# Optimization experiments

Hardware: AMD Instinct MI355X
Metric: run time of the kernel (lower is better)

The kernel has to match this reference:

```python
import jax, jax.numpy as jnp
import numpy as np
from jax import lax

EPS = 1e-5
DN = ('NCDHW', 'OIDHW', 'NCDHW')
CHANNELS = [4, 32, 64, 128, 256, 512]
OUT_CH = 256


def _conv_s2(x, w):
    # 3x3x3 conv, stride 2, padding 1 (torchsparse spnn.Conv3d on densified grid)
    return lax.conv_general_dilated(x, w, window_strides=(2, 2, 2),
                                    padding=[(1, 1)] * 3, dimension_numbers=DN)


def _bn_relu(x, g, b, m, v):
    # inference BatchNorm (running stats) + ReLU, fused elementwise
    inv = g * lax.rsqrt(v + EPS)           # [C]
    shp = (1, -1, 1, 1, 1)
    return jnp.maximum(x * inv.reshape(shp) + (b - m * inv).reshape(shp), 0.0)


def setup_inputs() -> dict:
    key = jax.random.key(0)
    ks = jax.random.split(key, 32)
    inp = {}
    inp['x'] = jax.random.normal(ks[0], (2, 4, 128, 128, 128), dtype=jnp.float32)
    ki = 1
    for i in range(5):
        cin, cout = CHANNELS[i], CHANNELS[i + 1]
        fan_in = cin * 27
        inp[f'w{i+1}'] = jax.random.normal(ks[ki], (cout, cin, 3, 3, 3), dtype=jnp.float32) / np.sqrt(fan_in); ki += 1
        inp[f'g{i+1}'] = 1.0 + 0.1 * jax.random.normal(ks[ki], (cout,), dtype=jnp.float32); ki += 1
        inp[f'b{i+1}'] = 0.1 * jax.random.normal(ks[ki], (cout,), dtype=jnp.float32); ki += 1
        inp[f'm{i+1}'] = 0.1 * jax.random.normal(ks[ki], (cout,), dtype=jnp.float32); ki += 1
        inp[f'v{i+1}'] = jax.random.uniform(ks[ki], (cout,), dtype=jnp.float32, minval=0.5, maxval=1.5); ki += 1
    inp['w_out'] = jax.random.normal(ks[ki], (OUT_CH, 512, 1, 1, 1), dtype=jnp.float32) / np.sqrt(512.0)
    return inp


def reference(x, w1, g1, b1, m1, v1, w2, g2, b2, m2, v2, w3, g3, b3, m3, v3,
              w4, g4, b4, m4, v4, w5, g5, b5, m5, v5, w_out):
    h = _bn_relu(_conv_s2(x, w1), g1, b1, m1, v1)   # [B,32,64,64,64]
    h = _bn_relu(_conv_s2(h, w2), g2, b2, m2, v2)   # [B,64,32,32,32]
    h = _bn_relu(_conv_s2(h, w3), g3, b3, m3, v3)   # [B,128,16,16,16]
    h = _bn_relu(_conv_s2(h, w4), g4, b4, m4, v4)   # [B,256,8,8,8]
    h = _bn_relu(_conv_s2(h, w5), g5, b5, m5, v5)   # [B,512,4,4,4]
    # 1x1x1 output conv, stride 1
    out = lax.conv_general_dilated(h, w_out, window_strides=(1, 1, 1),
                                   padding=[(0, 0)] * 3, dimension_numbers=DN)
    return out  # [B,256,4,4,4]
```

## Files before the change

kernel.cpp:

```cpp
#include <hip/hip_runtime.h>

static constexpr float kEps = 1e-5f;

using bf16x8 = __attribute__((ext_vector_type(8))) short;
using f32x4 = __attribute__((ext_vector_type(4))) float;
using f32x2 = __attribute__((ext_vector_type(2))) float;

constexpr int ilog2(int n) { return n <= 1 ? 0 : 1 + ilog2(n / 2); }

__device__ inline unsigned bf_rne(float v) {
  unsigned u = __float_as_uint(v);
  return (u + 0x7FFFu + ((u >> 16) & 1u)) >> 16;
}
__device__ inline void split_bf(float v, unsigned short& h, unsigned short& l) {
  unsigned hb = bf_rne(v);
  h = (unsigned short)hb;
  float hf = __uint_as_float(hb << 16);
  l = (unsigned short)bf_rne(v - hf);
}

__device__ inline void pk_fma(f32x2& d, f32x2 a, f32x2 b) {
  asm volatile("v_pk_fma_f32 %0, %1, %2, %0" : "+v"(d) : "v"(a), "v"(b));
}

__device__ inline void repack_s1_body(int idx, const float* __restrict__ w,
                                      const float* __restrict__ g,
                                      const float* __restrict__ b,
                                      const float* __restrict__ m,
                                      const float* __restrict__ v,
                                      float* __restrict__ wT,
                                      float* __restrict__ bias) {
  constexpr int CIN = 4, COUT = 32, total = COUT * CIN * 27;
  if (idx < COUT) {
    float inv = g[idx] * rsqrtf(v[idx] + kEps);
    bias[idx] = b[idx] - m[idx] * inv;
  }
  if (idx < total) {
    int cout = idx % COUT;
    int ck = idx / COUT;
    int cin = ck / 27;
    int k = ck % 27;
    float inv = g[cout] * rsqrtf(v[cout] + kEps);
    wT[idx] = w[(cout * CIN + cin) * 27 + k] * inv;
  }
}

template <int CIN, int COUT>
__device__ inline void repack_bf_body(int idx, const float* __restrict__ w,
                                      const float* __restrict__ g,
                                      const float* __restrict__ b,
                                      const float* __restrict__ m,
                                      const float* __restrict__ v,
                                      unsigned short* __restrict__ wh,
                                      unsigned short* __restrict__ wl,
                                      float* __restrict__ bias) {
  constexpr int total = 27 * COUT * CIN;
  constexpr int LC = ilog2(CIN), LO = ilog2(COUT);
  if (idx < COUT) {
    float inv = g[idx] * rsqrtf(v[idx] + kEps);
    bias[idx] = b[idx] - m[idx] * inv;
  }
  if (idx < total) {
    int ci = idx & (CIN - 1);
    int t = idx >> LC;
    int co = t & (COUT - 1);
    int tap = t >> LO;
    float inv = g[co] * rsqrtf(v[co] + kEps);
    float val = w[((size_t)co * CIN + ci) * 27 + tap] * inv;
    unsigned short h, l;
    split_bf(val, h, l);
    wh[idx] = h;
    wl[idx] = l;
  }
}

__global__ __launch_bounds__(256) void repack_all(
    const float* w1, const float* g1, const float* b1, const float* m1, const float* v1,
    const float* w2, const float* g2, const float* b2, const float* m2, const float* v2,
    const float* w3, const float* g3, const float* b3, const float* m3, const float* v3,
    const float* w4, const float* g4, const float* b4, const float* m4, const float* v4,
    const float* w5, const float* g5, const float* b5, const float* m5, const float* v5,
    const float* w_out, float* wt1, unsigned short* w2h, unsigned short* w2l,
    unsigned short* w3h, unsigned short* w3l, unsigned short* w4h, unsigned short* w4l,
    unsigned short* w5h, unsigned short* w5l, float* woutT, float* bs1, float* bs2,
    float* bs3, float* bs4, float* bs5) {
  int blk = blockIdx.x;
  int tid = threadIdx.x;
  if (blk < 14) {
    repack_s1_body(blk * 256 + tid, w1, g1, b1, m1, v1, wt1, bs1);
  } else if (blk < 230) {
    repack_bf_body<32, 64>((blk - 14) * 256 + tid, w2, g2, b2, m2, v2, w2h, w2l, bs2);
  } else if (blk < 1094) {
    repack_bf_body<64, 128>((blk - 230) * 256 + tid, w3, g3, b3, m3, v3, w3h, w3l, bs3);
  } else if (blk < 4550) {
    repack_bf_body<128, 256>((blk - 1094) * 256 + tid, w4, g4, b4, m4, v4, w4h, w4l, bs4);
  } else if (blk < 18374) {
    repack_bf_body<256, 512>((blk - 4550) * 256 + tid, w5, g5, b5, m5, v5, w5h, w5l, bs5);
  } else {
    int idx = (blk - 18374) * 256 + tid;
    int co = idx & 255;
    int c = idx >> 8;
    woutT[idx] = w_out[(size_t)co * 512 + c];
  }
}

__global__ __launch_bounds__(256) void conv1_direct(
    const float* __restrict__ in, const float* __restrict__ wT,
    const float* __restrict__ bias, unsigned short* __restrict__ outh,
    unsigned short* __restrict__ outl) {
  constexpr int DI = 128, CIN = 4, COUT = 32;
  int tid = blockIdx.x * 256 + threadIdx.x;
  int x = tid & 63;
  int t = tid >> 6;
  int y = t & 63;
  t >>= 6;
  int z = t & 63;
  int bb = t >> 6;

  f32x2 acc[16];
#pragma unroll
  for (int i = 0; i < 16; ++i) acc[i] = (f32x2){0.f, 0.f};

  const float* inb = in + (size_t)bb * CIN * DI * DI * DI;
  for (int cin = 0; cin < CIN; ++cin) {
    const float* inc = inb + (size_t)cin * DI * DI * DI;
#pragma unroll
    for (int kz = 0; kz < 3; ++kz) {
      int iz = 2 * z + kz - 1;
      if (iz < 0) continue;
#pragma unroll
      for (int ky = 0; ky < 3; ++ky) {
        int iy = 2 * y + ky - 1;
        if (iy < 0) continue;
        const float* row = inc + ((size_t)iz * DI + iy) * DI;
        f32x2 rv = *reinterpret_cast<const f32x2*>(row + 2 * x);
        float xm = (x > 0) ? row[2 * x - 1] : 0.f;
        const float* wbase = wT + ((size_t)cin * 27 + (kz * 3 + ky) * 3) * COUT;
        {
          f32x2 xv2 = (f32x2){xm, xm};
#pragma unroll
          for (int i = 0; i < 16; ++i)
            pk_fma(acc[i], *reinterpret_cast<const f32x2*>(wbase + 2 * i), xv2);
        }
        {
          f32x2 xv2 = (f32x2){rv.x, rv.x};
#pragma unroll
          for (int i = 0; i < 16; ++i)
            pk_fma(acc[i], *reinterpret_cast<const f32x2*>(wbase + COUT + 2 * i), xv2);
        }
        {
          f32x2 xv2 = (f32x2){rv.y, rv.y};
#pragma unroll
          for (int i = 0; i < 16; ++i)
            pk_fma(acc[i], *reinterpret_cast<const f32x2*>(wbase + 2 * COUT + 2 * i), xv2);
        }
      }
    }
  }
  int pidx = (z & 1) * 4 + (y & 1) * 2 + (x & 1);
  size_t sub = (((size_t)(z >> 1) * 32) + (y >> 1)) * 32 + (x >> 1);
  size_t op = (((size_t)bb * 8 + pidx) * 32768 + sub) * COUT;
#pragma unroll
  for (int i = 0; i < COUT; ++i) {
    float r = fmaxf(acc[i >> 1][i & 1] + bias[i], 0.f);
    unsigned short h, l;
    split_bf(r, h, l);
    outh[op + i] = h;
    outl[op + i] = l;
  }
}

template <int CIN, int COUT, int DO, int SK, int MREP>
__global__ __launch_bounds__(256) void conv_mfma(
    const unsigned short* __restrict__ inh, const unsigned short* __restrict__ inl,
    const unsigned short* __restrict__ wh, const unsigned short* __restrict__ wl,
    const float* __restrict__ bias, unsigned short* __restrict__ outh,
    unsigned short* __restrict__ outl, float* __restrict__ partial) {
  constexpr int M = 2 * DO * DO * DO;
  constexpr int TAPS = 27 / SK;
  constexpr int KCPT = CIN / 32;
  constexpr int LD = ilog2(DO);
  constexpr int SUB = DO * DO * DO;

  const int lane = threadIdx.x & 63;
  const int wv = threadIdx.x >> 6;
  const int mWave = (blockIdx.x * 4 + wv) * (MREP * 16);
  const int nBase = blockIdx.y * 64;
  const int skid = blockIdx.z;
  const int mlane = lane & 15;
  const int kgrp = lane >> 4;

  int xf[MREP], yf[MREP], zf[MREP], bf_[MREP];
#pragma unroll
  for (int f = 0; f < MREP; ++f) {
    int m = mWave + f * 16 + mlane;
    xf[f] = m & (DO - 1);
    yf[f] = (m >> LD) & (DO - 1);
    zf[f] = (m >> (2 * LD)) & (DO - 1);
    bf_[f] = m >> (3 * LD);
  }

  f32x4 acc[MREP][4];
#pragma unroll
  for (int f = 0; f < MREP; ++f)
#pragma unroll
    for (int q = 0; q < 4; ++q) acc[f][q] = (f32x4){0.f, 0.f, 0.f, 0.f};

  for (int tp = 0; tp < TAPS; ++tp) {
    const int tap = skid * TAPS + tp;
    const int kz = tap / 9;
    const int kr = tap - kz * 9;
    const int ky = kr / 3;
    const int kx = kr - ky * 3;
    const int pidx = (kz != 1) * 4 + (ky != 1) * 2 + (kx != 1);
    const int dz = (kz == 0), dy = (ky == 0), dx = (kx == 0);

    const size_t woff = (size_t)tap * COUT * CIN + (size_t)(nBase + mlane) * CIN + kgrp * 8;
    const unsigned short* wbh = wh + woff;
    const unsigned short* wbl = wl + woff;

    long long aoff[MREP];
    bool valid[MREP];
#pragma unroll
    for (int f = 0; f < MREP; ++f) {
      int sx = xf[f] - dx, sy = yf[f] - dy, sz = zf[f] - dz;
      valid[f] = ((sx | sy | sz) >= 0);
      aoff[f] = ((long long)(bf_[f] * 8 + pidx) * SUB + (sz * DO + sy) * DO + sx) * CIN +
                kgrp * 8;
    }

#pragma unroll
    for (int kc = 0; kc < KCPT; ++kc) {
      bf16x8 Ah[MREP], Al[MREP];
#pragma unroll
      for (int f = 0; f < MREP; ++f) {
        Ah[f] = (bf16x8){0, 0, 0, 0, 0, 0, 0, 0};
        Al[f] = (bf16x8){0, 0, 0, 0, 0, 0, 0, 0};
        if (valid[f]) {
          Ah[f] = *reinterpret_cast<const bf16x8*>(inh + aoff[f] + kc * 32);
          Al[f] = *reinterpret_cast<const bf16x8*>(inl + aoff[f] + kc * 32);
        }
      }
#pragma unroll
      for (int nq = 0; nq < 4; ++nq) {
        bf16x8 Bh = *reinterpret_cast<const bf16x8*>(wbh + (size_t)nq * 16 * CIN + kc * 32);
        bf16x8 Bl = *reinterpret_cast<const bf16x8*>(wbl + (size_t)nq * 16 * CIN + kc * 32);
#pragma unroll
        for (int f = 0; f < MREP; ++f) {
          acc[f][nq] = __builtin_amdgcn_mfma_f32_16x16x32_bf16(Ah[f], Bh, acc[f][nq], 0, 0, 0);
          acc[f][nq] = __builtin_amdgcn_mfma_f32_16x16x32_bf16(Ah[f], Bl, acc[f][nq], 0, 0, 0);
          acc[f][nq] = __builtin_amdgcn_mfma_f32_16x16x32_bf16(Al[f], Bh, acc[f][nq], 0, 0, 0);
        }
      }
    }
  }

  if constexpr (SK == 1) {
    constexpr int HD = DO / 2;
#pragma unroll
    for (int f = 0; f < MREP; ++f) {
#pragma unroll
      for (int nq = 0; nq < 4; ++nq) {
        const int n = nBase + nq * 16 + mlane;
        const float bv = bias[n];
#pragma unroll
        for (int r = 0; r < 4; ++r) {
          const int mrow = mWave + f * 16 + kgrp * 4 + r;
          const int ox = mrow & (DO - 1);
          const int oy = (mrow >> LD) & (DO - 1);
          const int oz = (mrow >> (2 * LD)) & (DO - 1);
          const int ob = mrow >> (3 * LD);
          const int pp = (oz & 1) * 4 + (oy & 1) * 2 + (ox & 1);
          const size_t sub = (((size_t)(oz >> 1) * HD) + (oy >> 1)) * HD + (ox >> 1);
          const size_t addr = (((size_t)ob * 8 + pp) * (HD * HD * HD) + sub) * COUT + n;
          float vv = fmaxf(acc[f][nq][r] + bv, 0.f);
          unsigned short h, l;
          split_bf(vv, h, l);
          outh[addr] = h;
          outl[addr] = l;
        }
      }
    }
  } else {
#pragma unroll
    for (int f = 0; f < MREP; ++f) {
#pragma unroll
      for (int nq = 0; nq < 4; ++nq) {
        const int n = nBase + nq * 16 + mlane;
#pragma unroll
        for (int r = 0; r < 4; ++r) {
          const int mrow = mWave + f * 16 + kgrp * 4 + r;
          partial[((size_t)skid * M + mrow) * COUT + n] = acc[f][nq][r];
        }
      }
    }
  }
}

template <int COUT, int SK, int M, int DOP>
__global__ __launch_bounds__(256) void reduce_split(
    const float* __restrict__ partial, const float* __restrict__ bias,
    unsigned short* __restrict__ oh, unsigned short* __restrict__ ol) {
  constexpr int LD = ilog2(DOP);
  constexpr int HD = DOP / 2;
  int idx = blockIdx.x * 256 + threadIdx.x;
  int n = idx & (COUT - 1);
  int mrow = idx / COUT;
  float s = 0.f;
#pragma unroll
  for (int k = 0; k < SK; ++k) s += partial[(size_t)k * M * COUT + idx];
  float v = fmaxf(s + bias[n], 0.f);
  const int ox = mrow & (DOP - 1);
  const int oy = (mrow >> LD) & (DOP - 1);
  const int oz = (mrow >> (2 * LD)) & (DOP - 1);
  const int ob = mrow >> (3 * LD);
  const int pp = (oz & 1) * 4 + (oy & 1) * 2 + (ox & 1);
  const size_t sub = (((size_t)(oz >> 1) * HD) + (oy >> 1)) * HD + (ox >> 1);
  const size_t addr = (((size_t)ob * 8 + pp) * (HD * HD * HD) + sub) * COUT + n;
  unsigned short h, l;
  split_bf(v, h, l);
  oh[addr] = h;
  ol[addr] = l;
}

__global__ __launch_bounds__(256) void final_fused(
    const float* __restrict__ p5, const float* __restrict__ bias,
    const float* __restrict__ wt, float* __restrict__ out) {
  __shared__ float h[512];
  int p = blockIdx.x;
  int t = threadIdx.x;
#pragma unroll
  for (int cc = 0; cc < 2; ++cc) {
    int c = t + cc * 256;
    float s = 0.f;
#pragma unroll
    for (int k = 0; k < 27; ++k) s += p5[((size_t)k * 128 + p) * 512 + c];
    h[c] = fmaxf(s + bias[c], 0.f);
  }
  __syncthreads();
  int b = p >> 6, sp = p & 63;
  float acc = 0.f;
#pragma unroll 8
  for (int c = 0; c < 512; ++c) acc = fmaf(h[c], wt[(size_t)c * 256 + t], acc);
  out[((size_t)b * 256 + t) * 64 + sp] = acc;
}

extern "C" void kernel_launch(void* const* d_in, const int* in_sizes, int n_in,
                              void* d_out, int out_size, void* d_ws,
                              size_t ws_size, hipStream_t stream) {
  const float* x = (const float*)d_in[0];
  const float* w1 = (const float*)d_in[1];
  const float* g1 = (const float*)d_in[2];
  const float* bb1 = (const float*)d_in[3];
  const float* m1 = (const float*)d_in[4];
  const float* v1 = (const float*)d_in[5];
  const float* w2 = (const float*)d_in[6];
  const float* g2 = (const float*)d_in[7];
  const float* bb2 = (const float*)d_in[8];
  const float* m2 = (const float*)d_in[9];
  const float* v2 = (const float*)d_in[10];
  const float* w3 = (const float*)d_in[11];
  const float* g3 = (const float*)d_in[12];
  const float* bb3 = (const float*)d_in[13];
  const float* m3 = (const float*)d_in[14];
  const float* v3 = (const float*)d_in[15];
  const float* w4 = (const float*)d_in[16];
  const float* g4 = (const float*)d_in[17];
  const float* bb4 = (const float*)d_in[18];
  const float* m4 = (const float*)d_in[19];
  const float* v4 = (const float*)d_in[20];
  const float* w5 = (const float*)d_in[21];
  const float* g5 = (const float*)d_in[22];
  const float* bb5 = (const float*)d_in[23];
  const float* m5 = (const float*)d_in[24];
  const float* v5 = (const float*)d_in[25];
  const float* w_out = (const float*)d_in[26];
  (void)in_sizes; (void)n_in; (void)out_size; (void)ws_size;

  char* base = (char*)d_ws;
  size_t off = 0;
  auto take = [&](size_t bytes) {
    char* p = base + off;
    off = (off + bytes + 255) & ~(size_t)255;
    return p;
  };
  float* wt1 = (float*)take(3456 * 4);
  unsigned short* w2h = (unsigned short*)take(55296 * 2);
  unsigned short* w2l = (unsigned short*)take(55296 * 2);
  unsigned short* w3h = (unsigned short*)take(221184 * 2);
  unsigned short* w3l = (unsigned short*)take(221184 * 2);
  unsigned short* w4h = (unsigned short*)take(884736 * 2);
  unsigned short* w4l = (unsigned short*)take(884736 * 2);
  unsigned short* w5h = (unsigned short*)take(3538944 * 2);
  unsigned short* w5l = (unsigned short*)take(3538944 * 2);
  float* woutT = (float*)take(131072 * 4);
  float* bs1 = (float*)take(32 * 4);
  float* bs2 = (float*)take(64 * 4);
  float* bs3 = (float*)take(128 * 4);
  float* bs4 = (float*)take(256 * 4);
  float* bs5 = (float*)take(512 * 4);
  unsigned short* h1h = (unsigned short*)take((size_t)16777216 * 2);
  unsigned short* h1l = (unsigned short*)take((size_t)16777216 * 2);
  unsigned short* h2h = (unsigned short*)take((size_t)4194304 * 2);
  unsigned short* h2l = (unsigned short*)take((size_t)4194304 * 2);

  char* AR = (char*)h1h;
  float* p3 = (float*)AR;
  float* p4 = (float*)AR;
  float* p5 = (float*)AR;
  char* AR2 = AR + ((size_t)16 << 20);
  unsigned short* h3h = (unsigned short*)AR2;
  unsigned short* h3l = (unsigned short*)(AR2 + 2097152);
  unsigned short* h4h = (unsigned short*)(AR2 + 2 * 2097152);
  unsigned short* h4l = (unsigned short*)(AR2 + 2 * 2097152 + 524288);

  repack_all<<<18886, 256, 0, stream>>>(
      w1, g1, bb1, m1, v1, w2, g2, bb2, m2, v2, w3, g3, bb3, m3, v3,
      w4, g4, bb4, m4, v4, w5, g5, bb5, m5, v5, w_out,
      wt1, w2h, w2l, w3h, w3l, w4h, w4l, w5h, w5l, woutT,
      bs1, bs2, bs3, bs4, bs5);

  conv1_direct<<<2048, 256, 0, stream>>>(x, wt1, bs1, h1h, h1l);

  conv_mfma<32, 64, 32, 1, 2><<<dim3(512, 1, 1), 256, 0, stream>>>(
      h1h, h1l, w2h, w2l, bs2, h2h, h2l, nullptr);

  conv_mfma<64, 128, 16, 3, 2><<<dim3(64, 2, 3), 256, 0, stream>>>(
      h2h, h2l, w3h, w3l, bs3, nullptr, nullptr, p3);
  reduce_split<128, 3, 8192, 16><<<4096, 256, 0, stream>>>(p3, bs3, h3h, h3l);

  conv_mfma<128, 256, 8, 9, 1><<<dim3(16, 4, 9), 256, 0, stream>>>(
      h3h, h3l, w4h, w4l, bs4, nullptr, nullptr, p4);
  reduce_split<256, 9, 1024, 8><<<1024, 256, 0, stream>>>(p4, bs4, h4h, h4l);

  conv_mfma<256, 512, 4, 27, 1><<<dim3(2, 8, 27), 256, 0, stream>>>(
      h4h, h4l, w5h, w5l, bs5, nullptr, nullptr, p5);

  final_fused<<<128, 256, 0, stream>>>(p5, bs5, woutT, (float*)d_out);
}
```

Before: 467.0 us.

## Use scalar FMAs in conv1 and retune MREP and split-K for conv2-4

The conv1 direct kernel drops its inline-asm packed FMA and uses plain scalar fmaf over 32 accumulators, with a per-tap x load. The MFMA convs for layers 2-4 get a larger MREP (more M tiles per block, so fewer blocks), and layer 3 changes split-K from 3 to 9 with a matching reduce. The partial-sum scratch region grows so h3/h4 are placed past the larger p3 buffer. These changes trade weight reuse per block against parallelism and partial-sum traffic, and conv1 now depends on the compiler's own FMA scheduling.

```diff
diff --git a/kernel.cpp b/kernel.cpp
--- a/kernel.cpp
+++ b/kernel.cpp
@@ -17,10 +17,6 @@
   h = (unsigned short)hb;
   float hf = __uint_as_float(hb << 16);
   l = (unsigned short)bf_rne(v - hf);
-}
-
-__device__ inline void pk_fma(f32x2& d, f32x2 a, f32x2 b) {
-  asm volatile("v_pk_fma_f32 %0, %1, %2, %0" : "+v"(d) : "v"(a), "v"(b));
 }
 
 __device__ inline void repack_s1_body(int idx, const float* __restrict__ w,
@@ -117,9 +113,9 @@
   int z = t & 63;
   int bb = t >> 6;
 
-  f32x2 acc[16];
-#pragma unroll
-  for (int i = 0; i < 16; ++i) acc[i] = (f32x2){0.f, 0.f};
+  float acc[COUT];
+#pragma unroll
+  for (int i = 0; i < COUT; ++i) acc[i] = 0.f;
 
   const float* inb = in + (size_t)bb * CIN * DI * DI * DI;
   for (int cin = 0; cin < CIN; ++cin) {
@@ -133,26 +129,13 @@
         int iy = 2 * y + ky - 1;
         if (iy < 0) continue;
         const float* row = inc + ((size_t)iz * DI + iy) * DI;
-        f32x2 rv = *reinterpret_cast<const f32x2*>(row + 2 * x);
-        float xm = (x > 0) ? row[2 * x - 1] : 0.f;
-        const float* wbase = wT + ((size_t)cin * 27 + (kz * 3 + ky) * 3) * COUT;
-        {
-          f32x2 xv2 = (f32x2){xm, xm};
-#pragma unroll
-          for (int i = 0; i < 16; ++i)
-            pk_fma(acc[i], *reinterpret_cast<const f32x2*>(wbase + 2 * i), xv2);
-        }
-        {
-          f32x2 xv2 = (f32x2){rv.x, rv.x};
-#pragma unroll
-          for (int i = 0; i < 16; ++i)
-            pk_fma(acc[i], *reinterpret_cast<const f32x2*>(wbase + COUT + 2 * i), xv2);
-        }
-        {
-          f32x2 xv2 = (f32x2){rv.y, rv.y};
-#pragma unroll
-          for (int i = 0; i < 16; ++i)
-            pk_fma(acc[i], *reinterpret_cast<const f32x2*>(wbase + 2 * COUT + 2 * i), xv2);
+#pragma unroll
+        for (int kx = 0; kx < 3; ++kx) {
+          int ix = 2 * x + kx - 1;
+          float xv = (ix >= 0) ? row[ix] : 0.f;
+          const float* wp = wT + ((size_t)cin * 27 + (kz * 3 + ky) * 3 + kx) * COUT;
+#pragma unroll
+          for (int i = 0; i < COUT; ++i) acc[i] = fmaf(xv, wp[i], acc[i]);
         }
       }
     }
@@ -162,7 +145,7 @@
   size_t op = (((size_t)bb * 8 + pidx) * 32768 + sub) * COUT;
 #pragma unroll
   for (int i = 0; i < COUT; ++i) {
-    float r = fmaxf(acc[i >> 1][i & 1] + bias[i], 0.f);
+    float r = fmaxf(acc[i] + bias[i], 0.f);
     unsigned short h, l;
     split_bf(r, h, l);
     outh[op + i] = h;
@@ -408,7 +391,7 @@
   float* p3 = (float*)AR;
   float* p4 = (float*)AR;
   float* p5 = (float*)AR;
-  char* AR2 = AR + ((size_t)16 << 20);
+  char* AR2 = AR + ((size_t)40 << 20);
   unsigned short* h3h = (unsigned short*)AR2;
   unsigned short* h3l = (unsigned short*)(AR2 + 2097152);
   unsigned short* h4h = (unsigned short*)(AR2 + 2 * 2097152);
@@ -422,14 +405,14 @@
 
   conv1_direct<<<2048, 256, 0, stream>>>(x, wt1, bs1, h1h, h1l);
 
-  conv_mfma<32, 64, 32, 1, 2><<<dim3(512, 1, 1), 256, 0, stream>>>(
+  conv_mfma<32, 64, 32, 1, 4><<<dim3(256, 1, 1), 256, 0, stream>>>(
       h1h, h1l, w2h, w2l, bs2, h2h, h2l, nullptr);
 
-  conv_mfma<64, 128, 16, 3, 2><<<dim3(64, 2, 3), 256, 0, stream>>>(
+  conv_mfma<64, 128, 16, 9, 4><<<dim3(32, 2, 9), 256, 0, stream>>>(
       h2h, h2l, w3h, w3l, bs3, nullptr, nullptr, p3);
-  reduce_split<128, 3, 8192, 16><<<4096, 256, 0, stream>>>(p3, bs3, h3h, h3l);
-
-  conv_mfma<128, 256, 8, 9, 1><<<dim3(16, 4, 9), 256, 0, stream>>>(
+  reduce_split<128, 9, 8192, 16><<<4096, 256, 0, stream>>>(p3, bs3, h3h, h3l);
+
+  conv_mfma<128, 256, 8, 9, 2><<<dim3(8, 4, 9), 256, 0, stream>>>(
       h3h, h3l, w4h, w4l, bs4, nullptr, nullptr, p4);
   reduce_split<256, 9, 1024, 8><<<1024, 256, 0, stream>>>(p4, bs4, h4h, h4l);
 
```

After: 379.7 us. 18.7% less time.
